# Performance work log

Measured on AMD Instinct MI355X. Metric: run time of the kernel, lower is better.

Reference implementation:

```python
import jax, jax.numpy as jnp
import numpy as np


def setup_inputs() -> dict:
    key = jax.random.key(0)
    k1, k2, k3 = jax.random.split(key, 3)
    B, S, D = 4, 4096, 2048
    a = jax.random.uniform(k1, (B, S, D), dtype=jnp.float32)   # decay coeffs in [0,1)
    b = jax.random.normal(k2, (B, S, D), dtype=jnp.float32)
    h0 = jax.random.normal(k3, (B, D), dtype=jnp.float32)
    return {"a": a, "b": b, "h0": h0}


def _scan(a, b):
    # Associative op for h_t = a_t * h_{t-1} + b_t:
    # combining left segment (a_l, b_l) then right segment (a_r, b_r)
    # gives (a_l * a_r, a_r * b_l + b_r).
    def combine(left, right):
        a_l, b_l = left
        a_r, b_r = right
        return a_l * a_r, a_r * b_l + b_r
    _, h = jax.lax.associative_scan(combine, (a, b), axis=1)
    return h  # (batch, seq_len, dim)


def reference(a, b, h0):
    # Fold initial state into first input term: b_0 <- b_0 + a_0 * h0
    b = b.at[:, 0, :].add(a[:, 0, :] * h0)
    return _scan(a, b)
```

## Files before the change

### kernel.cpp

```cpp
#include <hip/hip_runtime.h>

#define BATCH 4
#define SEQ   4096
#define DIM   2048
#define D4    (DIM / 4)
#define GQ    2
#define NCHAIN (BATCH * DIM)

typedef __attribute__((ext_vector_type(4))) float v4f;

template<int LSEG>
__global__ __launch_bounds__(256) void k1_aggregate(
    const float4* __restrict__ a4, const float4* __restrict__ b4,
    float4* __restrict__ aggA4, float4* __restrict__ aggB4)
{
    const int c     = blockIdx.x;
    const int gq    = blockIdx.y;
    const int batch = blockIdx.z;
    const int d4    = gq * 256 + threadIdx.x;

    unsigned base = (unsigned)(batch * SEQ + c * LSEG) * D4 + d4;

    float4 A = make_float4(1.f, 1.f, 1.f, 1.f);
    float4 B = make_float4(0.f, 0.f, 0.f, 0.f);

#pragma unroll 1
    for (int h = 0; h < LSEG / 8; ++h) {
        float4 av[8], bv[8];
        const unsigned hb = base + (unsigned)(h * 8) * D4;
#pragma unroll
        for (int i = 0; i < 8; ++i) av[i] = a4[hb + (unsigned)i * D4];
#pragma unroll
        for (int i = 0; i < 8; ++i) bv[i] = b4[hb + (unsigned)i * D4];
#pragma unroll
        for (int i = 0; i < 8; ++i) {
            B.x = fmaf(av[i].x, B.x, bv[i].x);  A.x *= av[i].x;
            B.y = fmaf(av[i].y, B.y, bv[i].y);  A.y *= av[i].y;
            B.z = fmaf(av[i].z, B.z, bv[i].z);  A.z *= av[i].z;
            B.w = fmaf(av[i].w, B.w, bv[i].w);  A.w *= av[i].w;
        }
    }
    const unsigned aidx = (unsigned)c * (NCHAIN / 4) + batch * (DIM / 4) + d4;
    aggA4[aidx] = A;
    aggB4[aidx] = B;
}

template<int NC>
__global__ __launch_bounds__(512) void k2_scan_agg(
    const float* __restrict__ aggA, const float* __restrict__ aggB,
    const float* __restrict__ h0, float* __restrict__ pref)
{
    constexpr int CPG = NC / 8;
    const int lc = threadIdx.x & 63;
    const int g  = threadIdx.x >> 6;
    const int ch = blockIdx.x * 64 + lc;

    const unsigned idx0 = (unsigned)(g * CPG) * NCHAIN + (unsigned)ch;

    float A = 1.f, B = 0.f;
#pragma unroll 8
    for (int i = 0; i < CPG; ++i) {
        const unsigned idx = idx0 + (unsigned)i * NCHAIN;
        const float a = aggA[idx];
        const float b = aggB[idx];
        B = fmaf(a, B, b);
        A *= a;
    }

    __shared__ float sA[8][64];
    __shared__ float sB[8][64];
    __shared__ float sH[8][64];
    sA[g][lc] = A;
    sB[g][lc] = B;
    __syncthreads();

    if (threadIdx.x < 64) {
        float h = h0[ch];
#pragma unroll
        for (int j = 0; j < 8; ++j) {
            sH[j][lc] = h;
            h = fmaf(sA[j][lc], h, sB[j][lc]);
        }
    }
    __syncthreads();

    float h = sH[g][lc];
#pragma unroll 8
    for (int i = 0; i < CPG; ++i) {
        const unsigned idx = idx0 + (unsigned)i * NCHAIN;
        pref[idx] = h;
        h = fmaf(aggA[idx], h, aggB[idx]);
    }
}

template<int LSEG>
__global__ __launch_bounds__(256) void k3_apply(
    const float4* __restrict__ a4, const float4* __restrict__ b4,
    const float4* __restrict__ pref4, float4* __restrict__ out4)
{
    const int c     = blockIdx.x;
    const int gq    = blockIdx.y;
    const int batch = blockIdx.z;
    const int d4    = gq * 256 + threadIdx.x;

    unsigned base = (unsigned)(batch * SEQ + c * LSEG) * D4 + d4;
    const unsigned aidx = (unsigned)c * (NCHAIN / 4) + batch * (DIM / 4) + d4;

    float4 h = pref4[aidx];

#pragma unroll 1
    for (int hh = 0; hh < LSEG / 8; ++hh) {
        float4 av[8], bv[8];
        const unsigned hb = base + (unsigned)(hh * 8) * D4;
#pragma unroll
        for (int i = 0; i < 8; ++i) av[i] = a4[hb + (unsigned)i * D4];
#pragma unroll
        for (int i = 0; i < 8; ++i) bv[i] = b4[hb + (unsigned)i * D4];
#pragma unroll
        for (int i = 0; i < 8; ++i) {
            h.x = fmaf(av[i].x, h.x, bv[i].x);
            h.y = fmaf(av[i].y, h.y, bv[i].y);
            h.z = fmaf(av[i].z, h.z, bv[i].z);
            h.w = fmaf(av[i].w, h.w, bv[i].w);
            __builtin_nontemporal_store(*(const v4f*)&h, (v4f*)&out4[hb + (unsigned)i * D4]);
        }
    }
}

__global__ void scan_naive_kernel(
    const float* __restrict__ a, const float* __restrict__ b,
    const float* __restrict__ h0, float* __restrict__ out)
{
    const int chain = blockIdx.x * blockDim.x + threadIdx.x;
    if (chain >= NCHAIN) return;
    const int batch = chain / DIM;
    const int dim = chain % DIM;
    float h = h0[batch * DIM + dim];
    unsigned idx = (unsigned)(batch * SEQ) * DIM + dim;
    for (int s = 0; s < SEQ; ++s, idx += DIM) {
        h = fmaf(a[idx], h, b[idx]);
        out[idx] = h;
    }
}

template<int LSEG>
static void run_path(const float* a, const float* b, const float* h0,
                     float* out, float* ws, hipStream_t stream)
{
    constexpr int NC = SEQ / LSEG;
    const size_t seg_vals = (size_t)NC * NCHAIN;
    float* aggA = ws;
    float* aggB = aggA + seg_vals;
    float* pref = aggB + seg_vals;

    k1_aggregate<LSEG><<<dim3(NC, GQ, BATCH), dim3(256), 0, stream>>>(
        (const float4*)a, (const float4*)b, (float4*)aggA, (float4*)aggB);
    k2_scan_agg<NC><<<dim3(NCHAIN / 64), dim3(512), 0, stream>>>(
        aggA, aggB, h0, pref);
    k3_apply<LSEG><<<dim3(NC, GQ, BATCH), dim3(256), 0, stream>>>(
        (const float4*)a, (const float4*)b, (const float4*)pref, (float4*)out);
}

extern "C" void kernel_launch(void* const* d_in, const int* in_sizes, int n_in,
                              void* d_out, int out_size, void* d_ws, size_t ws_size,
                              hipStream_t stream) {
    const float* a  = (const float*)d_in[0];
    const float* b  = (const float*)d_in[1];
    const float* h0 = (const float*)d_in[2];
    float* out = (float*)d_out;

    const size_t need16 = 3 * (size_t)(SEQ / 16) * NCHAIN * sizeof(float);
    const size_t need32 = 3 * (size_t)(SEQ / 32) * NCHAIN * sizeof(float);

    if (ws_size >= need16) {
        run_path<16>(a, b, h0, out, (float*)d_ws, stream);
    } else if (ws_size >= need32) {
        run_path<32>(a, b, h0, out, (float*)d_ws, stream);
    } else {
        scan_naive_kernel<<<dim3((NCHAIN + 255) / 256), dim3(256), 0, stream>>>(
            a, b, h0, out);
    }
}
```

Baseline: 369.3 us.

## Split aggregate pass per batch with alternating nontemporal loads to steer cache residency

The aggregate kernel is split into four per-batch launches. Batches 1 and 3 use nontemporal loads so their data does not evict cached lines, which is meant to leave batches 0 and 2 resident in L2/MALL for the apply pass that re-reads a and b. The inner loops are also rewritten from explicit batched 8-load register arrays to a simple unroll-8 loop. This adds three kernel launches and makes the amount of reuse depend on cache capacity.

After: 359.6 us. -2.6%, faster.

```diff
diff --git a/kernel.cpp b/kernel.cpp
--- a/kernel.cpp
+++ b/kernel.cpp
@@ -9,40 +9,52 @@
 
 typedef __attribute__((ext_vector_type(4))) float v4f;
 
-template<int LSEG>
-__global__ __launch_bounds__(256) void k1_aggregate(
+__device__ __forceinline__ float4 ld_nt(const float4* p) {
+    v4f v = __builtin_nontemporal_load((const v4f*)p);
+    return make_float4(v.x, v.y, v.z, v.w);
+}
+
+template<int LSEG, bool NT>
+__device__ __forceinline__ void k1_body(
     const float4* __restrict__ a4, const float4* __restrict__ b4,
-    float4* __restrict__ aggA4, float4* __restrict__ aggB4)
+    float4* __restrict__ aggA4, float4* __restrict__ aggB4, int batch)
 {
-    const int c     = blockIdx.x;
-    const int gq    = blockIdx.y;
-    const int batch = blockIdx.z;
-    const int d4    = gq * 256 + threadIdx.x;
+    const int c  = blockIdx.x;
+    const int gq = blockIdx.y;
+    const int d4 = gq * 256 + threadIdx.x;
 
     unsigned base = (unsigned)(batch * SEQ + c * LSEG) * D4 + d4;
 
     float4 A = make_float4(1.f, 1.f, 1.f, 1.f);
     float4 B = make_float4(0.f, 0.f, 0.f, 0.f);
-
-#pragma unroll 1
-    for (int h = 0; h < LSEG / 8; ++h) {
-        float4 av[8], bv[8];
-        const unsigned hb = base + (unsigned)(h * 8) * D4;
-#pragma unroll
-        for (int i = 0; i < 8; ++i) av[i] = a4[hb + (unsigned)i * D4];
-#pragma unroll
-        for (int i = 0; i < 8; ++i) bv[i] = b4[hb + (unsigned)i * D4];
-#pragma unroll
-        for (int i = 0; i < 8; ++i) {
-            B.x = fmaf(av[i].x, B.x, bv[i].x);  A.x *= av[i].x;
-            B.y = fmaf(av[i].y, B.y, bv[i].y);  A.y *= av[i].y;
-            B.z = fmaf(av[i].z, B.z, bv[i].z);  A.z *= av[i].z;
-            B.w = fmaf(av[i].w, B.w, bv[i].w);  A.w *= av[i].w;
-        }
+#pragma unroll 8
+    for (int t = 0; t < LSEG; ++t) {
+        const float4 av = NT ? ld_nt(&a4[base + (unsigned)t * D4]) : a4[base + (unsigned)t * D4];
+        const float4 bv = NT ? ld_nt(&b4[base + (unsigned)t * D4]) : b4[base + (unsigned)t * D4];
+        B.x = fmaf(av.x, B.x, bv.x);  A.x *= av.x;
+        B.y = fmaf(av.y, B.y, bv.y);  A.y *= av.y;
+        B.z = fmaf(av.z, B.z, bv.z);  A.z *= av.z;
+        B.w = fmaf(av.w, B.w, bv.w);  A.w *= av.w;
     }
     const unsigned aidx = (unsigned)c * (NCHAIN / 4) + batch * (DIM / 4) + d4;
     aggA4[aidx] = A;
     aggB4[aidx] = B;
+}
+
+template<int LSEG>
+__global__ __launch_bounds__(256) void k1_reg(
+    const float4* __restrict__ a4, const float4* __restrict__ b4,
+    float4* __restrict__ aggA4, float4* __restrict__ aggB4, int batch)
+{
+    k1_body<LSEG, false>(a4, b4, aggA4, aggB4, batch);
+}
+
+template<int LSEG>
+__global__ __launch_bounds__(256) void k1_nt(
+    const float4* __restrict__ a4, const float4* __restrict__ b4,
+    float4* __restrict__ aggA4, float4* __restrict__ aggB4, int batch)
+{
+    k1_body<LSEG, true>(a4, b4, aggA4, aggB4, batch);
 }
 
 template<int NC>
@@ -107,23 +119,15 @@
     const unsigned aidx = (unsigned)c * (NCHAIN / 4) + batch * (DIM / 4) + d4;
 
     float4 h = pref4[aidx];
-
-#pragma unroll 1
-    for (int hh = 0; hh < LSEG / 8; ++hh) {
-        float4 av[8], bv[8];
-        const unsigned hb = base + (unsigned)(hh * 8) * D4;
-#pragma unroll
-        for (int i = 0; i < 8; ++i) av[i] = a4[hb + (unsigned)i * D4];
-#pragma unroll
-        for (int i = 0; i < 8; ++i) bv[i] = b4[hb + (unsigned)i * D4];
-#pragma unroll
-        for (int i = 0; i < 8; ++i) {
-            h.x = fmaf(av[i].x, h.x, bv[i].x);
-            h.y = fmaf(av[i].y, h.y, bv[i].y);
-            h.z = fmaf(av[i].z, h.z, bv[i].z);
-            h.w = fmaf(av[i].w, h.w, bv[i].w);
-            __builtin_nontemporal_store(*(const v4f*)&h, (v4f*)&out4[hb + (unsigned)i * D4]);
-        }
+#pragma unroll 8
+    for (int t = 0; t < LSEG; ++t) {
+        const float4 av = a4[base + (unsigned)t * D4];
+        const float4 bv = b4[base + (unsigned)t * D4];
+        h.x = fmaf(av.x, h.x, bv.x);
+        h.y = fmaf(av.y, h.y, bv.y);
+        h.z = fmaf(av.z, h.z, bv.z);
+        h.w = fmaf(av.w, h.w, bv.w);
+        __builtin_nontemporal_store(*(const v4f*)&h, (v4f*)&out4[base + (unsigned)t * D4]);
     }
 }
 
@@ -153,8 +157,15 @@
     float* aggB = aggA + seg_vals;
     float* pref = aggB + seg_vals;
 
-    k1_aggregate<LSEG><<<dim3(NC, GQ, BATCH), dim3(256), 0, stream>>>(
-        (const float4*)a, (const float4*)b, (float4*)aggA, (float4*)aggB);
+    k1_reg<LSEG><<<dim3(NC, GQ, 1), dim3(256), 0, stream>>>(
+        (const float4*)a, (const float4*)b, (float4*)aggA, (float4*)aggB, 0);
+    k1_nt<LSEG><<<dim3(NC, GQ, 1), dim3(256), 0, stream>>>(
+        (const float4*)a, (const float4*)b, (float4*)aggA, (float4*)aggB, 1);
+    k1_reg<LSEG><<<dim3(NC, GQ, 1), dim3(256), 0, stream>>>(
+        (const float4*)a, (const float4*)b, (float4*)aggA, (float4*)aggB, 2);
+    k1_nt<LSEG><<<dim3(NC, GQ, 1), dim3(256), 0, stream>>>(
+        (const float4*)a, (const float4*)b, (float4*)aggA, (float4*)aggB, 3);
+
     k2_scan_agg<NC><<<dim3(NCHAIN / 64), dim3(512), 0, stream>>>(
         aggA, aggB, h0, pref);
     k3_apply<LSEG><<<dim3(NC, GQ, BATCH), dim3(256), 0, stream>>>(
```
